# Performance work log

Hardware: AMD Instinct MI355X
Metric: run time of the kernel (lower is better)

Reference implementation:

```python
import jax, jax.numpy as jnp
import numpy as np

NODE_DIM = 64
OUT_DIM = 64
EDGE_DIM = 64
N_NODES = 50000
N_EDGES = 800000
BN_EPS = 1e-5


def _batchnorm(x, gamma, beta):
    # training-mode BatchNorm1d: biased batch statistics
    mean = jnp.mean(x, axis=0)
    var = jnp.mean((x - mean) ** 2, axis=0)
    return (x - mean) * jax.lax.rsqrt(var + BN_EPS) * gamma + beta


def setup_inputs() -> dict:
    key = jax.random.key(0)
    ks = jax.random.split(key, 16)
    s = 0.05  # weight init scale
    inp = {
        "em": jax.random.normal(ks[0], (N_NODES, NODE_DIM), jnp.float32),
        "edge_index": jax.random.randint(ks[1], (2, N_EDGES), 0, N_NODES, jnp.int64),
        "edge_features": jax.random.normal(ks[2], (N_EDGES, EDGE_DIM), jnp.float32),
        # GINEConv edge linear (edge_dim -> node_dim)
        "W_le": jax.random.normal(ks[3], (EDGE_DIM, NODE_DIM), jnp.float32) * s,
        "b_le": jnp.zeros((NODE_DIM,), jnp.float32),
        # GINEConv nn: Linear(node_dim, out) -> ReLU -> Linear(out, out)
        "W1": jax.random.normal(ks[4], (NODE_DIM, OUT_DIM), jnp.float32) * s,
        "b1": jnp.zeros((OUT_DIM,), jnp.float32),
        "W2": jax.random.normal(ks[5], (OUT_DIM, OUT_DIM), jnp.float32) * s,
        "b2": jnp.zeros((OUT_DIM,), jnp.float32),
        # x BatchNorm affine
        "gx": jnp.ones((OUT_DIM,), jnp.float32),
        "bx": jnp.zeros((OUT_DIM,), jnp.float32),
        # edge MLP: (edge_dim + 2*out) -> out -> out -> out
        "We1": jax.random.normal(ks[6], (EDGE_DIM + 2 * OUT_DIM, OUT_DIM), jnp.float32) * s,
        "be1": jnp.zeros((OUT_DIM,), jnp.float32),
        "We2": jax.random.normal(ks[7], (OUT_DIM, OUT_DIM), jnp.float32) * s,
        "be2": jnp.zeros((OUT_DIM,), jnp.float32),
        "We3": jax.random.normal(ks[8], (OUT_DIM, OUT_DIM), jnp.float32) * s,
        "be3": jnp.zeros((OUT_DIM,), jnp.float32),
        # edge BatchNorm affine
        "ge": jnp.ones((OUT_DIM,), jnp.float32),
        "be": jnp.zeros((OUT_DIM,), jnp.float32),
    }
    return inp


def reference(em, edge_index, edge_features, W_le, b_le, W1, b1, W2, b2, gx, bx,
              We1, be1, We2, be2, We3, be3, ge, be):
    src, dst = edge_index[0], edge_index[1]
    # GINEConv: msg = relu(x_j + lin(edge_attr)), sum-aggregated at target
    msg = jax.nn.relu(em[src] + edge_features @ W_le + b_le)  # [E, node_dim]
    aggr = jax.ops.segment_sum(msg, dst, num_segments=em.shape[0])  # [N, node_dim]
    h = em + aggr  # eps = 0
    h = jax.nn.relu(h @ W1 + b1) @ W2 + b2  # [N, out]
    x_em = jax.nn.relu(_batchnorm(h, gx, bx))
    # edge update: concat(x_em[src], x_em[dst], edge_features)
    edge_mess = jnp.concatenate([x_em[src], x_em[dst], edge_features], axis=1)
    e = jax.nn.relu(edge_mess @ We1 + be1)
    e = jax.nn.relu(e @ We2 + be2)
    e = e @ We3 + be3
    edge_out = jax.nn.relu(_batchnorm(e, ge, be))
    return x_em, edge_out
```

## Files before the change

kernel.cpp:

```cpp
#include <hip/hip_runtime.h>
#include <cstddef>

#define NN 50000
#define NE 800000

typedef __bf16 bf16x8 __attribute__((ext_vector_type(8)));
typedef float  f32x4  __attribute__((ext_vector_type(4)));

__device__ __forceinline__ bf16x8 ldfrag(const __bf16* __restrict__ wfr, int f, int lane) {
    return *reinterpret_cast<const bf16x8*>(wfr + (size_t)(f * 64 + lane) * 8);
}
__device__ __forceinline__ f32x4 mfma16(bf16x8 a, bf16x8 b, f32x4 c) {
    return __builtin_amdgcn_mfma_f32_16x16x32_bf16(a, b, c, 0, 0, 0);
}
__device__ __forceinline__ bool idx_is64(const int* eidx) {
    return ((eidx[1] | eidx[3] | eidx[5] | eidx[7]) == 0);
}
__device__ __forceinline__ int ld_src(const int* eidx, bool is64, int e) {
    return is64 ? eidx[(size_t)2 * e] : eidx[e];
}
__device__ __forceinline__ int ld_dst(const int* eidx, bool is64, int e) {
    return is64 ? eidx[2 * ((size_t)NE + e)] : eidx[(size_t)NE + e];
}
__device__ __forceinline__ bf16x8 cvt8(const float* __restrict__ p) {
    float4 v0 = *reinterpret_cast<const float4*>(p);
    float4 v1 = *reinterpret_cast<const float4*>(p + 4);
    bf16x8 r;
    r[0] = (__bf16)v0.x; r[1] = (__bf16)v0.y; r[2] = (__bf16)v0.z; r[3] = (__bf16)v0.w;
    r[4] = (__bf16)v1.x; r[5] = (__bf16)v1.y; r[6] = (__bf16)v1.z; r[7] = (__bf16)v1.w;
    return r;
}

__global__ __launch_bounds__(256) void prep(const float* __restrict__ wle, const float* __restrict__ w1,
                                            const float* __restrict__ w2, const float* __restrict__ we1,
                                            const float* __restrict__ we2, const float* __restrict__ we3,
                                            __bf16* __restrict__ wfr) {
    int sid = blockIdx.x * 256 + threadIdx.x;
    int f = sid >> 6, lane = sid & 63;
    const float* W; int fo;
    if (f < 8)       { W = wle; fo = 0; }
    else if (f < 16) { W = w1;  fo = 8; }
    else if (f < 24) { W = w2;  fo = 16; }
    else if (f < 48) { W = we1; fo = 24; }
    else if (f < 56) { W = we2; fo = 48; }
    else             { W = we3; fo = 56; }
    int lf = f - fo, kt = lf >> 2, nt = lf & 3;
    int g = lane >> 4, c = lane & 15;
#pragma unroll
    for (int b = 0; b < 8; b++) {
        int k = kt * 32 + g * 8 + b;
        int n = nt * 16 + c;
        wfr[(size_t)(f * 64 + lane) * 8 + b] = (__bf16)W[(size_t)k * 64 + n];
    }
}

__global__ __launch_bounds__(256) void k1(const float* __restrict__ em, const int* __restrict__ eidx,
                                          const float* __restrict__ ef, const __bf16* __restrict__ wfr,
                                          const float* __restrict__ ble, float* __restrict__ nodebuf,
                                          __bf16* __restrict__ ef16) {
    const int t = threadIdx.x;
    const int base = blockIdx.x * 64;
    const int lane = t & 63, w = t >> 6, c = lane & 15, g = lane >> 4;
    const int erow = base + w * 16 + c;
    const bool is64 = idx_is64(eidx);
    bf16x8 a[2];
#pragma unroll
    for (int kt = 0; kt < 2; kt++) {
        a[kt] = cvt8(ef + (size_t)erow * 64 + kt * 32 + g * 8);
        if (ef16) *reinterpret_cast<bf16x8*>(ef16 + (size_t)erow * 64 + kt * 32 + g * 8) = a[kt];
    }
    f32x4 acc[4] = {{0.f,0.f,0.f,0.f},{0.f,0.f,0.f,0.f},{0.f,0.f,0.f,0.f},{0.f,0.f,0.f,0.f}};
#pragma unroll
    for (int kt = 0; kt < 2; kt++)
#pragma unroll
        for (int nt = 0; nt < 4; nt++) acc[nt] = mfma16(a[kt], ldfrag(wfr, kt * 4 + nt, lane), acc[nt]);
#pragma unroll
    for (int rr = 0; rr < 4; rr++) {
        int e = base + w * 16 + g * 4 + rr;
        int sn = ld_src(eidx, is64, e);
        int dn = ld_dst(eidx, is64, e);
#pragma unroll
        for (int nt = 0; nt < 4; nt++) {
            int col = nt * 16 + c;
            float v = acc[nt][rr] + ble[col] + em[(size_t)sn * 64 + col];
            if (v > 0.f) atomicAdd(&nodebuf[(size_t)dn * 64 + col], v);
        }
    }
}

__global__ __launch_bounds__(256) void k2(const float* __restrict__ em, float* __restrict__ nb,
                                          const __bf16* __restrict__ wfr, const float* __restrict__ b1,
                                          const float* __restrict__ b2, float* __restrict__ sums) {
    __shared__ __bf16 Ysh[64][72];
    __shared__ float bs[128];
    const int t = threadIdx.x;
    const int base = blockIdx.x * 64;
    if (t < 128) bs[t] = 0.f;
    __syncthreads();
    const int lane = t & 63, w = t >> 6, c = lane & 15, g = lane >> 4;
    const int arow = base + w * 16 + c;
    const size_t rl = (size_t)(arow < NN ? arow : NN - 1) * 64;
    bf16x8 a[2];
#pragma unroll
    for (int kt = 0; kt < 2; kt++) {
        int off = kt * 32 + g * 8;
        float4 e0 = *reinterpret_cast<const float4*>(em + rl + off);
        float4 e1 = *reinterpret_cast<const float4*>(em + rl + off + 4);
        float4 n0 = *reinterpret_cast<const float4*>(nb + rl + off);
        float4 n1 = *reinterpret_cast<const float4*>(nb + rl + off + 4);
        bf16x8 r;
        r[0] = (__bf16)(e0.x + n0.x); r[1] = (__bf16)(e0.y + n0.y);
        r[2] = (__bf16)(e0.z + n0.z); r[3] = (__bf16)(e0.w + n0.w);
        r[4] = (__bf16)(e1.x + n1.x); r[5] = (__bf16)(e1.y + n1.y);
        r[6] = (__bf16)(e1.z + n1.z); r[7] = (__bf16)(e1.w + n1.w);
        a[kt] = r;
    }
    f32x4 a1[4] = {{0.f,0.f,0.f,0.f},{0.f,0.f,0.f,0.f},{0.f,0.f,0.f,0.f},{0.f,0.f,0.f,0.f}};
#pragma unroll
    for (int kt = 0; kt < 2; kt++)
#pragma unroll
        for (int nt = 0; nt < 4; nt++) a1[nt] = mfma16(a[kt], ldfrag(wfr, 8 + kt * 4 + nt, lane), a1[nt]);
#pragma unroll
    for (int nt = 0; nt < 4; nt++) {
        float bb = b1[nt * 16 + c];
#pragma unroll
        for (int rr = 0; rr < 4; rr++) {
            float v = a1[nt][rr] + bb;
            v = v > 0.f ? v : 0.f;
            Ysh[w * 16 + g * 4 + rr][nt * 16 + c] = (__bf16)v;
        }
    }
    bf16x8 ya[2];
#pragma unroll
    for (int kt = 0; kt < 2; kt++)
        ya[kt] = *reinterpret_cast<const bf16x8*>(&Ysh[w * 16 + c][kt * 32 + g * 8]);
    f32x4 a2[4] = {{0.f,0.f,0.f,0.f},{0.f,0.f,0.f,0.f},{0.f,0.f,0.f,0.f},{0.f,0.f,0.f,0.f}};
#pragma unroll
    for (int kt = 0; kt < 2; kt++)
#pragma unroll
        for (int nt = 0; nt < 4; nt++) a2[nt] = mfma16(ya[kt], ldfrag(wfr, 16 + kt * 4 + nt, lane), a2[nt]);
#pragma unroll
    for (int nt = 0; nt < 4; nt++) {
        int col = nt * 16 + c;
        float bb = b2[col];
        float ss = 0.f, qq = 0.f;
#pragma unroll
        for (int rr = 0; rr < 4; rr++) {
            int row = base + w * 16 + g * 4 + rr;
            if (row < NN) {
                float v = a2[nt][rr] + bb;
                nb[(size_t)row * 64 + col] = v;
                ss += v; qq += v * v;
            }
        }
        ss += __shfl_xor(ss, 16); ss += __shfl_xor(ss, 32);
        qq += __shfl_xor(qq, 16); qq += __shfl_xor(qq, 32);
        if (g == 0) { atomicAdd(&bs[col], ss); atomicAdd(&bs[64 + col], qq); }
    }
    __syncthreads();
    if (t < 128) atomicAdd(&sums[t], bs[t]);
}

__global__ __launch_bounds__(256) void k3(float* __restrict__ nb, const float* __restrict__ sums,
                                          const float* __restrict__ gx, const float* __restrict__ bx,
                                          __bf16* __restrict__ wsx) {
    size_t i4 = (size_t)(blockIdx.x * 256 + threadIdx.x) * 4;
    int col0 = (int)(i4 & 63);
    float4 v = *reinterpret_cast<const float4*>(nb + i4);
    const float* pv = reinterpret_cast<const float*>(&v);
    float o[4]; short so[4];
#pragma unroll
    for (int j = 0; j < 4; j++) {
        int col = col0 + j;
        float m   = sums[col] * (1.0f / 50000.0f);
        float var = sums[64 + col] * (1.0f / 50000.0f) - m * m;
        float inv = rsqrtf(var + 1e-5f);
        float x = (pv[j] - m) * inv * gx[col] + bx[col];
        x = x > 0.f ? x : 0.f;
        o[j] = x;
        so[j] = __builtin_bit_cast(short, (__bf16)x);
    }
    *reinterpret_cast<float4*>(nb + i4) = make_float4(o[0], o[1], o[2], o[3]);
    *reinterpret_cast<short4*>(wsx + i4) = make_short4(so[0], so[1], so[2], so[3]);
}

__global__ __launch_bounds__(256) void k4(const int* __restrict__ eidx, const float* __restrict__ ef,
                                          const __bf16* __restrict__ ef16, const __bf16* __restrict__ wsx,
                                          const __bf16* __restrict__ wfr,
                                          const float* __restrict__ be1, const float* __restrict__ be2,
                                          const float* __restrict__ be3, float* __restrict__ eout,
                                          float* __restrict__ pws) {
    __shared__ __bf16 Ysh[64][72];
    __shared__ float bs[128];
    const int t = threadIdx.x;
    const int base = blockIdx.x * 64;
    if (t < 128) bs[t] = 0.f;
    __syncthreads();
    const int lane = t & 63, w = t >> 6, c = lane & 15, g = lane >> 4;
    const int erow = base + w * 16 + c;
    const bool is64 = idx_is64(eidx);
    const int sn = ld_src(eidx, is64, erow);
    const int dn = ld_dst(eidx, is64, erow);
    bf16x8 xs[2], xd[2], ea[2];
#pragma unroll
    for (int kt = 0; kt < 2; kt++) {
        int off = kt * 32 + g * 8;
        xs[kt] = *reinterpret_cast<const bf16x8*>(wsx + (size_t)sn * 64 + off);
        xd[kt] = *reinterpret_cast<const bf16x8*>(wsx + (size_t)dn * 64 + off);
        ea[kt] = ef16 ? *reinterpret_cast<const bf16x8*>(ef16 + (size_t)erow * 64 + off)
                      : cvt8(ef + (size_t)erow * 64 + off);
    }
    f32x4 a1[4] = {{0.f,0.f,0.f,0.f},{0.f,0.f,0.f,0.f},{0.f,0.f,0.f,0.f},{0.f,0.f,0.f,0.f}};
#pragma unroll
    for (int kt = 0; kt < 2; kt++)
#pragma unroll
        for (int nt = 0; nt < 4; nt++) a1[nt] = mfma16(xs[kt], ldfrag(wfr, 24 + kt * 4 + nt, lane), a1[nt]);
#pragma unroll
    for (int kt = 0; kt < 2; kt++)
#pragma unroll
        for (int nt = 0; nt < 4; nt++) a1[nt] = mfma16(xd[kt], ldfrag(wfr, 32 + kt * 4 + nt, lane), a1[nt]);
#pragma unroll
    for (int kt = 0; kt < 2; kt++)
#pragma unroll
        for (int nt = 0; nt < 4; nt++) a1[nt] = mfma16(ea[kt], ldfrag(wfr, 40 + kt * 4 + nt, lane), a1[nt]);
#pragma unroll
    for (int nt = 0; nt < 4; nt++) {
        float bb = be1[nt * 16 + c];
#pragma unroll
        for (int rr = 0; rr < 4; rr++) {
            float v = a1[nt][rr] + bb;
            v = v > 0.f ? v : 0.f;
            Ysh[w * 16 + g * 4 + rr][nt * 16 + c] = (__bf16)v;
        }
    }
    bf16x8 ya[2];
#pragma unroll
    for (int kt = 0; kt < 2; kt++)
        ya[kt] = *reinterpret_cast<const bf16x8*>(&Ysh[w * 16 + c][kt * 32 + g * 8]);
    f32x4 a2[4] = {{0.f,0.f,0.f,0.f},{0.f,0.f,0.f,0.f},{0.f,0.f,0.f,0.f},{0.f,0.f,0.f,0.f}};
#pragma unroll
    for (int kt = 0; kt < 2; kt++)
#pragma unroll
        for (int nt = 0; nt < 4; nt++) a2[nt] = mfma16(ya[kt], ldfrag(wfr, 48 + kt * 4 + nt, lane), a2[nt]);
#pragma unroll
    for (int nt = 0; nt < 4; nt++) {
        float bb = be2[nt * 16 + c];
#pragma unroll
        for (int rr = 0; rr < 4; rr++) {
            float v = a2[nt][rr] + bb;
            v = v > 0.f ? v : 0.f;
            Ysh[w * 16 + g * 4 + rr][nt * 16 + c] = (__bf16)v;
        }
    }
#pragma unroll
    for (int kt = 0; kt < 2; kt++)
        ya[kt] = *reinterpret_cast<const bf16x8*>(&Ysh[w * 16 + c][kt * 32 + g * 8]);
    f32x4 a3[4] = {{0.f,0.f,0.f,0.f},{0.f,0.f,0.f,0.f},{0.f,0.f,0.f,0.f},{0.f,0.f,0.f,0.f}};
#pragma unroll
    for (int kt = 0; kt < 2; kt++)
#pragma unroll
        for (int nt = 0; nt < 4; nt++) a3[nt] = mfma16(ya[kt], ldfrag(wfr, 56 + kt * 4 + nt, lane), a3[nt]);
#pragma unroll
    for (int nt = 0; nt < 4; nt++) {
        int col = nt * 16 + c;
        float bb = be3[col];
        float ss = 0.f, qq = 0.f;
#pragma unroll
        for (int rr = 0; rr < 4; rr++) {
            int e = base + w * 16 + g * 4 + rr;
            float v = a3[nt][rr] + bb;
            eout[(size_t)e * 64 + col] = v;
            ss += v; qq += v * v;
        }
        ss += __shfl_xor(ss, 16); ss += __shfl_xor(ss, 32);
        qq += __shfl_xor(qq, 16); qq += __shfl_xor(qq, 32);
        if (g == 0) { atomicAdd(&bs[col], ss); atomicAdd(&bs[64 + col], qq); }
    }
    __syncthreads();
    if (t < 128) pws[(size_t)t * 12500 + blockIdx.x] = bs[t];
}

__global__ __launch_bounds__(256) void k4r(const float* __restrict__ pws, float* __restrict__ sums) {
    int b = blockIdx.x;
    float s = 0.f;
    for (int i = threadIdx.x; i < 12500; i += 256) s += pws[(size_t)b * 12500 + i];
#pragma unroll
    for (int m = 32; m >= 1; m >>= 1) s += __shfl_xor(s, m);
    __shared__ float acc4[4];
    int lane = threadIdx.x & 63, wid = threadIdx.x >> 6;
    if (lane == 0) acc4[wid] = s;
    __syncthreads();
    if (threadIdx.x == 0) sums[128 + b] = acc4[0] + acc4[1] + acc4[2] + acc4[3];
}

__global__ __launch_bounds__(256) void k5(float* __restrict__ eo, const float* __restrict__ sums,
                                          const float* __restrict__ ge, const float* __restrict__ be) {
    size_t i4 = (size_t)(blockIdx.x * 256 + threadIdx.x) * 4;
    int col0 = (int)(i4 & 63);
    float4 v = *reinterpret_cast<const float4*>(eo + i4);
    const float* pv = reinterpret_cast<const float*>(&v);
    float o[4];
#pragma unroll
    for (int j = 0; j < 4; j++) {
        int col = col0 + j;
        float m   = sums[128 + col] * (1.0f / 800000.0f);
        float var = sums[192 + col] * (1.0f / 800000.0f) - m * m;
        float inv = rsqrtf(var + 1e-5f);
        float x = (pv[j] - m) * inv * ge[col] + be[col];
        o[j] = x > 0.f ? x : 0.f;
    }
    *reinterpret_cast<float4*>(eo + i4) = make_float4(o[0], o[1], o[2], o[3]);
}

extern "C" void kernel_launch(void* const* d_in, const int* in_sizes, int n_in,
                              void* d_out, int out_size, void* d_ws, size_t ws_size,
                              hipStream_t stream) {
    const float* em   = (const float*)d_in[0];
    const int*   eidx = (const int*)d_in[1];
    const float* ef   = (const float*)d_in[2];
    const float* b_le = (const float*)d_in[4];
    const float* b1   = (const float*)d_in[6];
    const float* b2   = (const float*)d_in[8];
    const float* gx   = (const float*)d_in[9];
    const float* bx   = (const float*)d_in[10];
    const float* be1  = (const float*)d_in[12];
    const float* be2  = (const float*)d_in[14];
    const float* be3  = (const float*)d_in[16];
    const float* ge   = (const float*)d_in[17];
    const float* be   = (const float*)d_in[18];

    float* out = (float*)d_out;
    float* nodebuf = out;
    float* eout = out + (size_t)NN * 64;

    float*  sums = (float*)d_ws;
    __bf16* wfr  = (__bf16*)((char*)d_ws + 1024);
    __bf16* wsx  = (__bf16*)((char*)d_ws + 1024 + 65536);
    float*  pws  = (float*)((char*)d_ws + 1024 + 65536 + (size_t)NN * 64 * 2);
    size_t  base_need = 1024 + 65536 + (size_t)NN * 64 * 2 + (size_t)128 * 12500 * 4;
    __bf16* ef16 = (ws_size >= base_need + (size_t)NE * 64 * 2)
                   ? (__bf16*)((char*)d_ws + base_need) : nullptr;

    hipMemsetAsync(sums, 0, 256 * sizeof(float), stream);
    hipMemsetAsync(nodebuf, 0, (size_t)NN * 64 * sizeof(float), stream);

    prep<<<16, 256, 0, stream>>>((const float*)d_in[3], (const float*)d_in[5], (const float*)d_in[7],
                                 (const float*)d_in[11], (const float*)d_in[13], (const float*)d_in[15], wfr);
    k1<<<NE / 64, 256, 0, stream>>>(em, eidx, ef, wfr, b_le, nodebuf, ef16);
    k2<<<(NN + 63) / 64, 256, 0, stream>>>(em, nodebuf, wfr, b1, b2, sums);
    k3<<<(NN * 64) / 1024, 256, 0, stream>>>(nodebuf, sums, gx, bx, wsx);
    k4<<<NE / 64, 256, 0, stream>>>(eidx, ef, ef16, wsx, wfr, be1, be2, be3, eout, pws);
    k4r<<<128, 256, 0, stream>>>(pws, sums);
    k5<<<((size_t)NE * 64) / 1024, 256, 0, stream>>>(eout, sums, ge, be);
}
```

Before: 519.1 us.

## Shard scatter-add atomics across eight node buffers and drop the bf16 edge-feature cache

```diff
diff --git a/kernel.cpp b/kernel.cpp
--- a/kernel.cpp
+++ b/kernel.cpp
@@ -1,8 +1,10 @@
 #include <hip/hip_runtime.h>
 #include <cstddef>
+#include <cstdint>
 
 #define NN 50000
 #define NE 800000
+#define NSHARD 8
 
 typedef __bf16 bf16x8 __attribute__((ext_vector_type(8)));
 typedef float  f32x4  __attribute__((ext_vector_type(4)));
@@ -56,19 +58,17 @@
 
 __global__ __launch_bounds__(256) void k1(const float* __restrict__ em, const int* __restrict__ eidx,
                                           const float* __restrict__ ef, const __bf16* __restrict__ wfr,
-                                          const float* __restrict__ ble, float* __restrict__ nodebuf,
-                                          __bf16* __restrict__ ef16) {
+                                          const float* __restrict__ ble, float* __restrict__ shards) {
     const int t = threadIdx.x;
     const int base = blockIdx.x * 64;
     const int lane = t & 63, w = t >> 6, c = lane & 15, g = lane >> 4;
     const int erow = base + w * 16 + c;
     const bool is64 = idx_is64(eidx);
+    float* sh = shards + (size_t)(blockIdx.x & (NSHARD - 1)) * NN * 64;
     bf16x8 a[2];
 #pragma unroll
-    for (int kt = 0; kt < 2; kt++) {
+    for (int kt = 0; kt < 2; kt++)
         a[kt] = cvt8(ef + (size_t)erow * 64 + kt * 32 + g * 8);
-        if (ef16) *reinterpret_cast<bf16x8*>(ef16 + (size_t)erow * 64 + kt * 32 + g * 8) = a[kt];
-    }
     f32x4 acc[4] = {{0.f,0.f,0.f,0.f},{0.f,0.f,0.f,0.f},{0.f,0.f,0.f,0.f},{0.f,0.f,0.f,0.f}};
 #pragma unroll
     for (int kt = 0; kt < 2; kt++)
@@ -79,12 +79,26 @@
         int e = base + w * 16 + g * 4 + rr;
         int sn = ld_src(eidx, is64, e);
         int dn = ld_dst(eidx, is64, e);
+        float* nrow = sh + (size_t)dn * 64;
 #pragma unroll
         for (int nt = 0; nt < 4; nt++) {
             int col = nt * 16 + c;
             float v = acc[nt][rr] + ble[col] + em[(size_t)sn * 64 + col];
-            if (v > 0.f) atomicAdd(&nodebuf[(size_t)dn * 64 + col], v);
-        }
+            if (v > 0.f) atomicAdd(nrow + col, v);
+        }
+    }
+}
+
+__global__ __launch_bounds__(256) void k1r(const float* __restrict__ shards, float* __restrict__ nodebuf) {
+    const size_t total = (size_t)NN * 64 / 4;
+    for (size_t i = (size_t)blockIdx.x * 256 + threadIdx.x; i < total; i += (size_t)gridDim.x * 256) {
+        float sx = 0.f, sy = 0.f, sz = 0.f, sw = 0.f;
+#pragma unroll
+        for (int r = 0; r < NSHARD; r++) {
+            float4 v = *reinterpret_cast<const float4*>(shards + (size_t)r * NN * 64 + i * 4);
+            sx += v.x; sy += v.y; sz += v.z; sw += v.w;
+        }
+        *reinterpret_cast<float4*>(nodebuf + i * 4) = make_float4(sx, sy, sz, sw);
     }
 }
 
@@ -185,8 +199,7 @@
 }
 
 __global__ __launch_bounds__(256) void k4(const int* __restrict__ eidx, const float* __restrict__ ef,
-                                          const __bf16* __restrict__ ef16, const __bf16* __restrict__ wsx,
-                                          const __bf16* __restrict__ wfr,
+                                          const __bf16* __restrict__ wsx, const __bf16* __restrict__ wfr,
                                           const float* __restrict__ be1, const float* __restrict__ be2,
                                           const float* __restrict__ be3, float* __restrict__ eout,
                                           float* __restrict__ pws) {
@@ -207,8 +220,7 @@
         int off = kt * 32 + g * 8;
         xs[kt] = *reinterpret_cast<const bf16x8*>(wsx + (size_t)sn * 64 + off);
         xd[kt] = *reinterpret_cast<const bf16x8*>(wsx + (size_t)dn * 64 + off);
-        ea[kt] = ef16 ? *reinterpret_cast<const bf16x8*>(ef16 + (size_t)erow * 64 + off)
-                      : cvt8(ef + (size_t)erow * 64 + off);
+        ea[kt] = cvt8(ef + (size_t)erow * 64 + off);
     }
     f32x4 a1[4] = {{0.f,0.f,0.f,0.f},{0.f,0.f,0.f,0.f},{0.f,0.f,0.f,0.f},{0.f,0.f,0.f,0.f}};
 #pragma unroll
@@ -333,23 +345,22 @@
     float* nodebuf = out;
     float* eout = out + (size_t)NN * 64;
 
-    float*  sums = (float*)d_ws;
-    __bf16* wfr  = (__bf16*)((char*)d_ws + 1024);
-    __bf16* wsx  = (__bf16*)((char*)d_ws + 1024 + 65536);
-    float*  pws  = (float*)((char*)d_ws + 1024 + 65536 + (size_t)NN * 64 * 2);
-    size_t  base_need = 1024 + 65536 + (size_t)NN * 64 * 2 + (size_t)128 * 12500 * 4;
-    __bf16* ef16 = (ws_size >= base_need + (size_t)NE * 64 * 2)
-                   ? (__bf16*)((char*)d_ws + base_need) : nullptr;
+    float*  sums   = (float*)d_ws;
+    __bf16* wfr    = (__bf16*)((char*)d_ws + 1024);
+    __bf16* wsx    = (__bf16*)((char*)d_ws + 1024 + 65536);
+    float*  pws    = (float*)((char*)d_ws + 1024 + 65536 + (size_t)NN * 64 * 2);
+    float*  shards = (float*)((char*)d_ws + 1024 + 65536 + (size_t)NN * 64 * 2 + (size_t)128 * 12500 * 4);
 
     hipMemsetAsync(sums, 0, 256 * sizeof(float), stream);
-    hipMemsetAsync(nodebuf, 0, (size_t)NN * 64 * sizeof(float), stream);
+    hipMemsetAsync(shards, 0, (size_t)NSHARD * NN * 64 * sizeof(float), stream);
 
     prep<<<16, 256, 0, stream>>>((const float*)d_in[3], (const float*)d_in[5], (const float*)d_in[7],
                                  (const float*)d_in[11], (const float*)d_in[13], (const float*)d_in[15], wfr);
-    k1<<<NE / 64, 256, 0, stream>>>(em, eidx, ef, wfr, b_le, nodebuf, ef16);
+    k1<<<NE / 64, 256, 0, stream>>>(em, eidx, ef, wfr, b_le, shards);
+    k1r<<<1600, 256, 0, stream>>>(shards, nodebuf);
     k2<<<(NN + 63) / 64, 256, 0, stream>>>(em, nodebuf, wfr, b1, b2, sums);
     k3<<<(NN * 64) / 1024, 256, 0, stream>>>(nodebuf, sums, gx, bx, wsx);
-    k4<<<NE / 64, 256, 0, stream>>>(eidx, ef, ef16, wsx, wfr, be1, be2, be3, eout, pws);
+    k4<<<NE / 64, 256, 0, stream>>>(eidx, ef, wsx, wfr, be1, be2, be3, eout, pws);
     k4r<<<128, 256, 0, stream>>>(pws, sums);
     k5<<<((size_t)NE * 64) / 1024, 256, 0, stream>>>(eout, sums, ge, be);
 }
```

After: 565.3 us. 1.09x slower.

## Drop bf16 edge-feature cache, stage k1 loads via LDS, double k4 tile

Applied to the files above, without the earlier changes.

```diff
diff --git a/kernel.cpp b/kernel.cpp
--- a/kernel.cpp
+++ b/kernel.cpp
@@ -1,5 +1,6 @@
 #include <hip/hip_runtime.h>
 #include <cstddef>
+#include <cstdint>
 
 #define NN 50000
 #define NE 800000
@@ -56,24 +57,32 @@
 
 __global__ __launch_bounds__(256) void k1(const float* __restrict__ em, const int* __restrict__ eidx,
                                           const float* __restrict__ ef, const __bf16* __restrict__ wfr,
-                                          const float* __restrict__ ble, float* __restrict__ nodebuf,
-                                          __bf16* __restrict__ ef16) {
+                                          const float* __restrict__ ble, float* __restrict__ nodebuf) {
+    __shared__ __bf16 Ash[64][72];
     const int t = threadIdx.x;
     const int base = blockIdx.x * 64;
+    {
+        const int r = t >> 2, seg = t & 3;
+        const float4* p = reinterpret_cast<const float4*>(ef + (size_t)(base + r) * 64 + seg * 16);
+#pragma unroll
+        for (int i = 0; i < 4; i++) {
+            float4 v = p[i];
+            int cb = seg * 16 + i * 4;
+            Ash[r][cb + 0] = (__bf16)v.x; Ash[r][cb + 1] = (__bf16)v.y;
+            Ash[r][cb + 2] = (__bf16)v.z; Ash[r][cb + 3] = (__bf16)v.w;
+        }
+    }
+    const bool is64 = idx_is64(eidx);
+    __syncthreads();
     const int lane = t & 63, w = t >> 6, c = lane & 15, g = lane >> 4;
-    const int erow = base + w * 16 + c;
-    const bool is64 = idx_is64(eidx);
-    bf16x8 a[2];
+    const int arow = w * 16 + c;
+    f32x4 acc[4] = {{0.f,0.f,0.f,0.f},{0.f,0.f,0.f,0.f},{0.f,0.f,0.f,0.f},{0.f,0.f,0.f,0.f}};
 #pragma unroll
     for (int kt = 0; kt < 2; kt++) {
-        a[kt] = cvt8(ef + (size_t)erow * 64 + kt * 32 + g * 8);
-        if (ef16) *reinterpret_cast<bf16x8*>(ef16 + (size_t)erow * 64 + kt * 32 + g * 8) = a[kt];
-    }
-    f32x4 acc[4] = {{0.f,0.f,0.f,0.f},{0.f,0.f,0.f,0.f},{0.f,0.f,0.f,0.f},{0.f,0.f,0.f,0.f}};
-#pragma unroll
-    for (int kt = 0; kt < 2; kt++)
-#pragma unroll
-        for (int nt = 0; nt < 4; nt++) acc[nt] = mfma16(a[kt], ldfrag(wfr, kt * 4 + nt, lane), acc[nt]);
+        bf16x8 a = *reinterpret_cast<const bf16x8*>(&Ash[arow][kt * 32 + g * 8]);
+#pragma unroll
+        for (int nt = 0; nt < 4; nt++) acc[nt] = mfma16(a, ldfrag(wfr, kt * 4 + nt, lane), acc[nt]);
+    }
 #pragma unroll
     for (int rr = 0; rr < 4; rr++) {
         int e = base + w * 16 + g * 4 + rr;
@@ -185,105 +194,140 @@
 }
 
 __global__ __launch_bounds__(256) void k4(const int* __restrict__ eidx, const float* __restrict__ ef,
-                                          const __bf16* __restrict__ ef16, const __bf16* __restrict__ wsx,
-                                          const __bf16* __restrict__ wfr,
+                                          const __bf16* __restrict__ wsx, const __bf16* __restrict__ wfr,
                                           const float* __restrict__ be1, const float* __restrict__ be2,
                                           const float* __restrict__ be3, float* __restrict__ eout,
                                           float* __restrict__ pws) {
-    __shared__ __bf16 Ysh[64][72];
+    __shared__ __bf16 Ysh[2][64][72];
     __shared__ float bs[128];
     const int t = threadIdx.x;
-    const int base = blockIdx.x * 64;
+    const int blockb = blockIdx.x * 128;
     if (t < 128) bs[t] = 0.f;
     __syncthreads();
     const int lane = t & 63, w = t >> 6, c = lane & 15, g = lane >> 4;
-    const int erow = base + w * 16 + c;
     const bool is64 = idx_is64(eidx);
-    const int sn = ld_src(eidx, is64, erow);
-    const int dn = ld_dst(eidx, is64, erow);
-    bf16x8 xs[2], xd[2], ea[2];
-#pragma unroll
-    for (int kt = 0; kt < 2; kt++) {
-        int off = kt * 32 + g * 8;
-        xs[kt] = *reinterpret_cast<const bf16x8*>(wsx + (size_t)sn * 64 + off);
-        xd[kt] = *reinterpret_cast<const bf16x8*>(wsx + (size_t)dn * 64 + off);
-        ea[kt] = ef16 ? *reinterpret_cast<const bf16x8*>(ef16 + (size_t)erow * 64 + off)
-                      : cvt8(ef + (size_t)erow * 64 + off);
-    }
-    f32x4 a1[4] = {{0.f,0.f,0.f,0.f},{0.f,0.f,0.f,0.f},{0.f,0.f,0.f,0.f},{0.f,0.f,0.f,0.f}};
-#pragma unroll
-    for (int kt = 0; kt < 2; kt++)
-#pragma unroll
-        for (int nt = 0; nt < 4; nt++) a1[nt] = mfma16(xs[kt], ldfrag(wfr, 24 + kt * 4 + nt, lane), a1[nt]);
-#pragma unroll
-    for (int kt = 0; kt < 2; kt++)
-#pragma unroll
-        for (int nt = 0; nt < 4; nt++) a1[nt] = mfma16(xd[kt], ldfrag(wfr, 32 + kt * 4 + nt, lane), a1[nt]);
-#pragma unroll
-    for (int kt = 0; kt < 2; kt++)
-#pragma unroll
-        for (int nt = 0; nt < 4; nt++) a1[nt] = mfma16(ea[kt], ldfrag(wfr, 40 + kt * 4 + nt, lane), a1[nt]);
-#pragma unroll
-    for (int nt = 0; nt < 4; nt++) {
-        float bb = be1[nt * 16 + c];
-#pragma unroll
-        for (int rr = 0; rr < 4; rr++) {
-            float v = a1[nt][rr] + bb;
-            v = v > 0.f ? v : 0.f;
-            Ysh[w * 16 + g * 4 + rr][nt * 16 + c] = (__bf16)v;
-        }
-    }
-    bf16x8 ya[2];
-#pragma unroll
-    for (int kt = 0; kt < 2; kt++)
-        ya[kt] = *reinterpret_cast<const bf16x8*>(&Ysh[w * 16 + c][kt * 32 + g * 8]);
-    f32x4 a2[4] = {{0.f,0.f,0.f,0.f},{0.f,0.f,0.f,0.f},{0.f,0.f,0.f,0.f},{0.f,0.f,0.f,0.f}};
-#pragma unroll
-    for (int kt = 0; kt < 2; kt++)
-#pragma unroll
-        for (int nt = 0; nt < 4; nt++) a2[nt] = mfma16(ya[kt], ldfrag(wfr, 48 + kt * 4 + nt, lane), a2[nt]);
-#pragma unroll
-    for (int nt = 0; nt < 4; nt++) {
-        float bb = be2[nt * 16 + c];
-#pragma unroll
-        for (int rr = 0; rr < 4; rr++) {
-            float v = a2[nt][rr] + bb;
-            v = v > 0.f ? v : 0.f;
-            Ysh[w * 16 + g * 4 + rr][nt * 16 + c] = (__bf16)v;
-        }
-    }
-#pragma unroll
-    for (int kt = 0; kt < 2; kt++)
-        ya[kt] = *reinterpret_cast<const bf16x8*>(&Ysh[w * 16 + c][kt * 32 + g * 8]);
-    f32x4 a3[4] = {{0.f,0.f,0.f,0.f},{0.f,0.f,0.f,0.f},{0.f,0.f,0.f,0.f},{0.f,0.f,0.f,0.f}};
-#pragma unroll
-    for (int kt = 0; kt < 2; kt++)
-#pragma unroll
-        for (int nt = 0; nt < 4; nt++) a3[nt] = mfma16(ya[kt], ldfrag(wfr, 56 + kt * 4 + nt, lane), a3[nt]);
-#pragma unroll
-    for (int nt = 0; nt < 4; nt++) {
-        int col = nt * 16 + c;
-        float bb = be3[col];
-        float ss = 0.f, qq = 0.f;
-#pragma unroll
-        for (int rr = 0; rr < 4; rr++) {
-            int e = base + w * 16 + g * 4 + rr;
-            float v = a3[nt][rr] + bb;
-            eout[(size_t)e * 64 + col] = v;
-            ss += v; qq += v * v;
-        }
-        ss += __shfl_xor(ss, 16); ss += __shfl_xor(ss, 32);
-        qq += __shfl_xor(qq, 16); qq += __shfl_xor(qq, 32);
-        if (g == 0) { atomicAdd(&bs[col], ss); atomicAdd(&bs[64 + col], qq); }
-    }
-    __syncthreads();
-    if (t < 128) pws[(size_t)t * 12500 + blockIdx.x] = bs[t];
+
+    int erow[2], sn[2], dn[2];
+    bf16x8 xs[2][2], xd[2][2], ea[2][2];
+#pragma unroll
+    for (int tt = 0; tt < 2; tt++) {
+        erow[tt] = blockb + tt * 64 + w * 16 + c;
+        sn[tt] = ld_src(eidx, is64, erow[tt]);
+        dn[tt] = ld_dst(eidx, is64, erow[tt]);
+#pragma unroll
+        for (int kt = 0; kt < 2; kt++) {
+            int off = kt * 32 + g * 8;
+            xs[tt][kt] = *reinterpret_cast<const bf16x8*>(wsx + (size_t)sn[tt] * 64 + off);
+            xd[tt][kt] = *reinterpret_cast<const bf16x8*>(wsx + (size_t)dn[tt] * 64 + off);
+            ea[tt][kt] = cvt8(ef + (size_t)erow[tt] * 64 + off);
+        }
+    }
+    f32x4 a1[2][4];
+#pragma unroll
+    for (int tt = 0; tt < 2; tt++)
+#pragma unroll
+        for (int nt = 0; nt < 4; nt++) a1[tt][nt] = f32x4{0.f,0.f,0.f,0.f};
+#pragma unroll
+    for (int tt = 0; tt < 2; tt++)
+#pragma unroll
+        for (int kt = 0; kt < 2; kt++)
+#pragma unroll
+            for (int nt = 0; nt < 4; nt++) a1[tt][nt] = mfma16(xs[tt][kt], ldfrag(wfr, 24 + kt * 4 + nt, lane), a1[tt][nt]);
+#pragma unroll
+    for (int tt = 0; tt < 2; tt++)
+#pragma unroll
+        for (int kt = 0; kt < 2; kt++)
+#pragma unroll
+            for (int nt = 0; nt < 4; nt++) a1[tt][nt] = mfma16(xd[tt][kt], ldfrag(wfr, 32 + kt * 4 + nt, lane), a1[tt][nt]);
+#pragma unroll
+    for (int tt = 0; tt < 2; tt++)
+#pragma unroll
+        for (int kt = 0; kt < 2; kt++)
+#pragma unroll
+            for (int nt = 0; nt < 4; nt++) a1[tt][nt] = mfma16(ea[tt][kt], ldfrag(wfr, 40 + kt * 4 + nt, lane), a1[tt][nt]);
+#pragma unroll
+    for (int tt = 0; tt < 2; tt++)
+#pragma unroll
+        for (int nt = 0; nt < 4; nt++) {
+            float bb = be1[nt * 16 + c];
+#pragma unroll
+            for (int rr = 0; rr < 4; rr++) {
+                float v = a1[tt][nt][rr] + bb;
+                v = v > 0.f ? v : 0.f;
+                Ysh[tt][w * 16 + g * 4 + rr][nt * 16 + c] = (__bf16)v;
+            }
+        }
+    bf16x8 ya[2][2];
+#pragma unroll
+    for (int tt = 0; tt < 2; tt++)
+#pragma unroll
+        for (int kt = 0; kt < 2; kt++)
+            ya[tt][kt] = *reinterpret_cast<const bf16x8*>(&Ysh[tt][w * 16 + c][kt * 32 + g * 8]);
+    f32x4 a2[2][4];
+#pragma unroll
+    for (int tt = 0; tt < 2; tt++)
+#pragma unroll
+        for (int nt = 0; nt < 4; nt++) a2[tt][nt] = f32x4{0.f,0.f,0.f,0.f};
+#pragma unroll
+    for (int tt = 0; tt < 2; tt++)
+#pragma unroll
+        for (int kt = 0; kt < 2; kt++)
+#pragma unroll
+            for (int nt = 0; nt < 4; nt++) a2[tt][nt] = mfma16(ya[tt][kt], ldfrag(wfr, 48 + kt * 4 + nt, lane), a2[tt][nt]);
+#pragma unroll
+    for (int tt = 0; tt < 2; tt++)
+#pragma unroll
+        for (int nt = 0; nt < 4; nt++) {
+            float bb = be2[nt * 16 + c];
+#pragma unroll
+            for (int rr = 0; rr < 4; rr++) {
+                float v = a2[tt][nt][rr] + bb;
+                v = v > 0.f ? v : 0.f;
+                Ysh[tt][w * 16 + g * 4 + rr][nt * 16 + c] = (__bf16)v;
+            }
+        }
+#pragma unroll
+    for (int tt = 0; tt < 2; tt++)
+#pragma unroll
+        for (int kt = 0; kt < 2; kt++)
+            ya[tt][kt] = *reinterpret_cast<const bf16x8*>(&Ysh[tt][w * 16 + c][kt * 32 + g * 8]);
+    f32x4 a3[2][4];
+#pragma unroll
+    for (int tt = 0; tt < 2; tt++)
+#pragma unroll
+        for (int nt = 0; nt < 4; nt++) a3[tt][nt] = f32x4{0.f,0.f,0.f,0.f};
+#pragma unroll
+    for (int tt = 0; tt < 2; tt++)
+#pragma unroll
+        for (int kt = 0; kt < 2; kt++)
+#pragma unroll
+            for (int nt = 0; nt < 4; nt++) a3[tt][nt] = mfma16(ya[tt][kt], ldfrag(wfr, 56 + kt * 4 + nt, lane), a3[tt][nt]);
+#pragma unroll
+    for (int tt = 0; tt < 2; tt++)
+#pragma unroll
+        for (int nt = 0; nt < 4; nt++) {
+            int col = nt * 16 + c;
+            float bb = be3[col];
+            float ss = 0.f, qq = 0.f;
+#pragma unroll
+            for (int rr = 0; rr < 4; rr++) {
+                int e = blockb + tt * 64 + w * 16 + g * 4 + rr;
+                float v = a3[tt][nt][rr] + bb;
+                eout[(size_t)e * 64 + col] = v;
+                ss += v; qq += v * v;
+            }
+            ss += __shfl_xor(ss, 16); ss += __shfl_xor(ss, 32);
+            qq += __shfl_xor(qq, 16); qq += __shfl_xor(qq, 32);
+            if (g == 0) { atomicAdd(&bs[col], ss); atomicAdd(&bs[64 + col], qq); }
+        }
+    __syncthreads();
+    if (t < 128) pws[(size_t)t * (NE / 128) + blockIdx.x] = bs[t];
 }
 
 __global__ __launch_bounds__(256) void k4r(const float* __restrict__ pws, float* __restrict__ sums) {
     int b = blockIdx.x;
     float s = 0.f;
-    for (int i = threadIdx.x; i < 12500; i += 256) s += pws[(size_t)b * 12500 + i];
+    for (int i = threadIdx.x; i < NE / 128; i += 256) s += pws[(size_t)b * (NE / 128) + i];
 #pragma unroll
     for (int m = 32; m >= 1; m >>= 1) s += __shfl_xor(s, m);
     __shared__ float acc4[4];
@@ -337,19 +381,16 @@
     __bf16* wfr  = (__bf16*)((char*)d_ws + 1024);
     __bf16* wsx  = (__bf16*)((char*)d_ws + 1024 + 65536);
     float*  pws  = (float*)((char*)d_ws + 1024 + 65536 + (size_t)NN * 64 * 2);
-    size_t  base_need = 1024 + 65536 + (size_t)NN * 64 * 2 + (size_t)128 * 12500 * 4;
-    __bf16* ef16 = (ws_size >= base_need + (size_t)NE * 64 * 2)
-                   ? (__bf16*)((char*)d_ws + base_need) : nullptr;
 
     hipMemsetAsync(sums, 0, 256 * sizeof(float), stream);
     hipMemsetAsync(nodebuf, 0, (size_t)NN * 64 * sizeof(float), stream);
 
     prep<<<16, 256, 0, stream>>>((const float*)d_in[3], (const float*)d_in[5], (const float*)d_in[7],
                                  (const float*)d_in[11], (const float*)d_in[13], (const float*)d_in[15], wfr);
-    k1<<<NE / 64, 256, 0, stream>>>(em, eidx, ef, wfr, b_le, nodebuf, ef16);
+    k1<<<NE / 64, 256, 0, stream>>>(em, eidx, ef, wfr, b_le, nodebuf);
     k2<<<(NN + 63) / 64, 256, 0, stream>>>(em, nodebuf, wfr, b1, b2, sums);
     k3<<<(NN * 64) / 1024, 256, 0, stream>>>(nodebuf, sums, gx, bx, wsx);
-    k4<<<NE / 64, 256, 0, stream>>>(eidx, ef, ef16, wsx, wfr, be1, be2, be3, eout, pws);
+    k4<<<NE / 128, 256, 0, stream>>>(eidx, ef, wsx, wfr, be1, be2, be3, eout, pws);
     k4r<<<128, 256, 0, stream>>>(pws, sums);
     k5<<<((size_t)NE * 64) / 1024, 256, 0, stream>>>(eout, sums, ge, be);
 }
```

Result: faster. 473.7 us (-8.7%).
